# Performance work log

Hardware: AMD Instinct MI355X
Metric: run time of the kernel (lower is better)

The kernel has to match this reference:

```python
import jax, jax.numpy as jnp
import numpy as np

T, B, NN = 20, 4, 500            # timesteps, batch, nodes per sample
M = B * NN                        # big-batched node count = 2000
IN_D, H, H2, OUT = 2, 128, 64, 32


def setup_inputs() -> dict:
    key = jax.random.key(0)
    ks = jax.random.split(key, 16)
    positions = jax.random.normal(ks[0], (T, M, IN_D), jnp.float32)
    adjacency = (jax.random.uniform(ks[1], (T, M, M)) < 0.01).astype(jnp.float32)
    adjacency = adjacency * (1.0 - jnp.eye(M, dtype=jnp.float32))
    ego_mask = jax.random.bernoulli(ks[2], 0.8, (B, T, NN))
    s = lambda k, shp, fan: (jax.random.normal(k, shp, jnp.float32) / np.sqrt(fan)).astype(jnp.float32)
    return {
        'positions': positions,
        'adjacency': adjacency,
        'ego_mask': ego_mask,
        'W1': s(ks[3], (IN_D, H), IN_D), 'b1': jnp.zeros((H,), jnp.float32),
        'W2': s(ks[4], (H, H), H),       'b2': jnp.zeros((H,), jnp.float32),
        'W_ih': s(ks[5], (4 * H, H), H), 'W_hh': s(ks[6], (4 * H, H), H),
        'b_ih': jnp.zeros((4 * H,), jnp.float32), 'b_hh': jnp.zeros((4 * H,), jnp.float32),
        'fc1_w': s(ks[7], (H, H2), H),   'fc1_b': jnp.zeros((H2,), jnp.float32),
        'fc2_w': s(ks[8], (H2, OUT), H2), 'fc2_b': jnp.zeros((OUT,), jnp.float32),
    }


def _forward(positions, adjacency, ego_mask, W1, b1, W2, b2,
             W_ih, W_hh, b_ih, b_hh, fc1_w, fc1_b, fc2_w, fc2_b):
    # ego_mask [B,T,NN] -> [T, B*NN] (matches permute(1,0,2).reshape(T,-1))
    mask = jnp.transpose(ego_mask, (1, 0, 2)).reshape(T, M).astype(positions.dtype)

    def gcn_timestep(x_t, a_t, m_t):
        # masked subgraph + self loops on kept nodes (PyG GCNConv normalization)
        Ahat = a_t * m_t[:, None] * m_t[None, :] + jnp.diag(m_t)   # [M,M]
        deg = Ahat.sum(axis=0)                                      # in-degree (col sum)
        dinv = jnp.where(deg > 0, jax.lax.rsqrt(jnp.maximum(deg, 1e-12)), 0.0)
        An = dinv[:, None] * Ahat * dinv[None, :]                   # D^-1/2 Ahat D^-1/2
        h1 = jax.nn.relu(An.T @ (x_t @ W1) + b1)                    # GCN1 + relu
        h2 = (An.T @ (h1 @ W2) + b2) * m_t[:, None]                 # GCN2, scatter into zeros
        return h2

    placeholder = jax.vmap(gcn_timestep)(positions, adjacency, mask)  # [T, M, H]

    # torch nn.LSTM (batch_first=False) on placeholder.transpose(0,1):
    # sequence axis = nodes (M), batch axis = T
    xs = jnp.transpose(placeholder, (1, 0, 2))  # [M, T, H]

    def lstm_step(carry, x_s):
        h, c = carry
        gates = x_s @ W_ih.T + b_ih + h @ W_hh.T + b_hh
        i, f, g, o = jnp.split(gates, 4, axis=-1)
        c = jax.nn.sigmoid(f) * c + jax.nn.sigmoid(i) * jnp.tanh(g)
        h = jax.nn.sigmoid(o) * jnp.tanh(c)
        return (h, c), h

    init = (jnp.zeros((T, H), positions.dtype), jnp.zeros((T, H), positions.dtype))
    _, lstm_out = jax.lax.scan(lstm_step, init, xs)  # [M, T, H]

    emb = lstm_out.reshape(B, NN, T, H)              # view(B, max_nodes, T, H)
    emb = jax.nn.relu(emb @ fc1_w + fc1_b)
    return emb @ fc2_w + fc2_b                       # [B, NN, T, OUT]


def reference(positions, adjacency, ego_mask, W1, b1, W2, b2,
              W_ih, W_hh, b_ih, b_hh, fc1_w, fc1_b, fc2_w, fc2_b):
    return _forward(positions, adjacency, ego_mask, W1, b1, W2, b2,
                    W_ih, W_hh, b_ih, b_hh, fc1_w, fc1_b, fc2_w, fc2_b)
```

## Files before the change

kernel.cpp:

```cpp
#include <hip/hip_runtime.h>
#include <hip/hip_bf16.h>

#define T_   20
#define B_   4
#define NN_  500
#define M_   2000
#define TM_  40000
#define H_   128
#define G_   512
#define H2_  64
#define OUT_ 32
#define ECAP 64
#define TG_  (T_ * G_)

typedef unsigned short ushort_t;
typedef unsigned int   uint_t;
typedef _Float16       f16;
typedef f16 f16x2 __attribute__((ext_vector_type(2)));
typedef f16 f16x8 __attribute__((ext_vector_type(8)));
typedef float f32x4 __attribute__((ext_vector_type(4)));

#if defined(__has_builtin)
#  if __has_builtin(__builtin_amdgcn_fdot2)
#    define HAVE_FDOT2 1
#  endif
#endif

__device__ inline float fdot2_(f16x2 a, f16x2 b, float c) {
#ifdef HAVE_FDOT2
    return __builtin_amdgcn_fdot2(a, b, c, false);
#else
    return c + (float)a.x * (float)b.x + (float)a.y * (float)b.y;
#endif
}

__device__ inline float fast_sig(float x) {
    float e = __builtin_amdgcn_exp2f(x * -1.4426950408889634f);
    return __builtin_amdgcn_rcpf(1.f + e);
}
__device__ inline float fast_tanh(float x) {
    float e = __builtin_amdgcn_exp2f(x * 2.8853900817779268f);
    return 1.f - 2.f * __builtin_amdgcn_rcpf(e + 1.f);
}

#define BARRAW() asm volatile("s_barrier" ::: "memory")

#define DPPADD(v, ctrl)                                                       \
    do {                                                                      \
        int nb_ = __builtin_amdgcn_update_dpp(                                \
            0, __builtin_bit_cast(int, v), (ctrl), 0xF, 0xF, true);           \
        v += __builtin_bit_cast(float, nb_);                                  \
    } while (0)

__global__ __launch_bounds__(1024) void k0_mask(const void* __restrict__ ego,
                                                float* __restrict__ mf,
                                                int* __restrict__ ecnt) {
    __shared__ int fl[3];
    int tid = threadIdx.x;
    if (tid < 3) fl[tid] = 0;
    __syncthreads();
    const uint_t* dw = (const uint_t*)ego;
    int a = 0, b = 0, c = 0;
    for (int i = tid; i < 2500; i += 1024) {
        uint_t v = dw[i];
        bool isf32  = (v == 0x3F800000u);
        bool isbf16 = (v == 0x00003F80u) || (v == 0x3F803F80u);
        if (isf32)  a = 1;
        if (isbf16) b = 1;
        if (v > 1u && !isf32 && !isbf16) c = 1;
    }
    if (a) fl[0] = 1;
    if (b) fl[1] = 1;
    if (c) fl[2] = 1;
    __syncthreads();
    int mode;
    if (fl[1])      mode = 3;
    else if (fl[0]) mode = 2;
    else if (fl[2]) mode = 1;
    else            mode = 0;
    int e = blockIdx.x * 1024 + tid;
    if (e >= TM_) return;
    ecnt[e] = 0;
    int t = e / M_, i = e % M_;
    int bb = i / NN_, n = i % NN_;
    int src = (bb * T_ + t) * NN_ + n;
    bool on;
    if (mode == 0)      on = ((const int*)ego)[src] != 0;
    else if (mode == 1) on = ((const unsigned char*)ego)[src] != 0;
    else if (mode == 2) on = ((const float*)ego)[src] != 0.f;
    else                on = ((const ushort_t*)ego)[src] != 0;
    mf[e] = on ? 1.f : 0.f;
}

#define JSTRIP 200
__global__ void k1_scan(const float* __restrict__ adj, const float* __restrict__ mf,
                        int* __restrict__ ecnt, int* __restrict__ edges) {
    __shared__ float ms[JSTRIP];
    int t = blockIdx.y, j0 = blockIdx.z * JSTRIP;
    int i = blockIdx.x * 256 + threadIdx.x;
    for (int idx = threadIdx.x; idx < JSTRIP; idx += 256)
        ms[idx] = mf[t * M_ + j0 + idx];
    __syncthreads();
    if (i >= M_) return;
    if (mf[t * M_ + i] == 0.f) return;
    const float* ap = adj + (size_t)t * M_ * M_ + (size_t)j0 * M_ + i;
    int r = t * M_ + i;
    int* ep = edges + (size_t)r * ECAP;
#pragma unroll 8
    for (int jj = 0; jj < JSTRIP; ++jj) {
        float av = ap[(size_t)jj * M_];
        if (av != 0.f && ms[jj] != 0.f) {
            int pos = atomicAdd(&ecnt[r], 1);
            if (pos < ECAP) ep[pos] = j0 + jj;
        }
    }
}

__global__ void k2_y1(const float* __restrict__ pos, const float* __restrict__ W1,
                      const float* __restrict__ mf, const int* __restrict__ ecnt,
                      float* __restrict__ dinv, f16* __restrict__ Y1) {
    int gid = blockIdx.x * 256 + threadIdx.x;
    int r = gid >> 7, h = gid & 127;
    if (r >= TM_) return;
    float mr = mf[r];
    int cnt = ecnt[r];
    float dv = (mr != 0.f) ? __frsqrt_rn((float)(cnt + 1)) : 0.f;
    if (h == 0) dinv[r] = dv;
    float2 xy = ((const float2*)pos)[r];
    float v = xy.x * W1[h] + xy.y * W1[H_ + h];
    Y1[gid] = (f16)(dv * v);
}

__global__ __launch_bounds__(64) void k3_agg1(const f16* __restrict__ Y1,
        const float* __restrict__ dinv, const int* __restrict__ ecnt,
        const int* __restrict__ edges, const float* __restrict__ b1,
        f16* __restrict__ h1) {
    int r = blockIdx.x, q = threadIdx.x;
    int t = r / M_, base = t * M_;
    const uint_t* Yu = (const uint_t*)Y1;
    f16x2 sp = __builtin_bit_cast(f16x2, Yu[(size_t)r * 64 + q]);
    float a0 = (float)sp.x, a1 = (float)sp.y;
    int ec = ecnt[r]; if (ec > ECAP) ec = ECAP;
    const int4* ep4 = (const int4*)(edges + (size_t)r * ECAP);
    for (int e = 0; e < ec; e += 4) {
        int4 ix = ep4[e >> 2];
        int j1 = (e + 1 < ec) ? ix.y : ix.x;
        int j2 = (e + 2 < ec) ? ix.z : ix.x;
        int j3 = (e + 3 < ec) ? ix.w : ix.x;
        uint_t u0 = Yu[(size_t)(base + ix.x) * 64 + q];
        uint_t u1 = Yu[(size_t)(base + j1) * 64 + q];
        uint_t u2 = Yu[(size_t)(base + j2) * 64 + q];
        uint_t u3 = Yu[(size_t)(base + j3) * 64 + q];
        f16x2 p0 = __builtin_bit_cast(f16x2, u0);
        a0 += (float)p0.x; a1 += (float)p0.y;
        if (e + 1 < ec) { f16x2 p = __builtin_bit_cast(f16x2, u1); a0 += (float)p.x; a1 += (float)p.y; }
        if (e + 2 < ec) { f16x2 p = __builtin_bit_cast(f16x2, u2); a0 += (float)p.x; a1 += (float)p.y; }
        if (e + 3 < ec) { f16x2 p = __builtin_bit_cast(f16x2, u3); a0 += (float)p.x; a1 += (float)p.y; }
    }
    float dv = dinv[r];
    float o0 = dv * a0 + b1[2 * q];
    float o1 = dv * a1 + b1[2 * q + 1];
    f16x2 op; op.x = (f16)fmaxf(o0, 0.f); op.y = (f16)fmaxf(o1, 0.f);
    ((uint_t*)h1)[(size_t)r * 64 + q] = __builtin_bit_cast(uint_t, op);
}

__global__ __launch_bounds__(64) void k5_agg2(const f16* __restrict__ Y2,
        const float* __restrict__ dinv, const float* __restrict__ mf,
        const int* __restrict__ ecnt, const int* __restrict__ edges,
        const float* __restrict__ b2, f16* __restrict__ ph) {
    int r = blockIdx.x, q = threadIdx.x;
    int t = r / M_, base = t * M_;
    const uint_t* Yu = (const uint_t*)Y2;
    f16x2 sp = __builtin_bit_cast(f16x2, Yu[(size_t)r * 64 + q]);
    float a0 = (float)sp.x, a1 = (float)sp.y;
    int ec = ecnt[r]; if (ec > ECAP) ec = ECAP;
    const int4* ep4 = (const int4*)(edges + (size_t)r * ECAP);
    for (int e = 0; e < ec; e += 4) {
        int4 ix = ep4[e >> 2];
        int j1 = (e + 1 < ec) ? ix.y : ix.x;
        int j2 = (e + 2 < ec) ? ix.z : ix.x;
        int j3 = (e + 3 < ec) ? ix.w : ix.x;
        uint_t u0 = Yu[(size_t)(base + ix.x) * 64 + q];
        uint_t u1 = Yu[(size_t)(base + j1) * 64 + q];
        uint_t u2 = Yu[(size_t)(base + j2) * 64 + q];
        uint_t u3 = Yu[(size_t)(base + j3) * 64 + q];
        f16x2 p0 = __builtin_bit_cast(f16x2, u0);
        a0 += (float)p0.x; a1 += (float)p0.y;
        if (e + 1 < ec) { f16x2 p = __builtin_bit_cast(f16x2, u1); a0 += (float)p.x; a1 += (float)p.y; }
        if (e + 2 < ec) { f16x2 p = __builtin_bit_cast(f16x2, u2); a0 += (float)p.x; a1 += (float)p.y; }
        if (e + 3 < ec) { f16x2 p = __builtin_bit_cast(f16x2, u3); a0 += (float)p.x; a1 += (float)p.y; }
    }
    float dv = dinv[r], mr = mf[r];
    f16x2 op;
    op.x = (f16)((dv * a0 + b2[2 * q]) * mr);
    op.y = (f16)((dv * a1 + b2[2 * q + 1]) * mr);
    ((uint_t*)ph)[(size_t)r * 64 + q] = __builtin_bit_cast(uint_t, op);
}

#define ALD 136
__global__ __launch_bounds__(256) void kgemm_mfma(const f16* __restrict__ A,
        const float* __restrict__ Bw, int bTrans, int Ntot, int mode,
        const float* __restrict__ dinv, const float* __restrict__ ba,
        const float* __restrict__ bb, f16* __restrict__ Out) {
    __shared__ f16 As[64 * ALD];
    __shared__ f16 Bs[64 * ALD];
    int m0 = blockIdx.x * 64;
    int n0 = blockIdx.y * 64;
    int tid = threadIdx.x;
#pragma unroll
    for (int u = 0; u < 4; ++u) {
        int idx = u * 256 + tid;
        int row = idx >> 4, seg = idx & 15;
        *(f16x8*)&As[row * ALD + seg * 8] =
            *(const f16x8*)(A + (size_t)(m0 + row) * H_ + seg * 8);
    }
    if (bTrans) {
#pragma unroll
        for (int u = 0; u < 16; ++u) {
            int idx = u * 256 + tid;
            int n = idx >> 6, k2 = (idx & 63) * 2;
            float2 v = *(const float2*)(Bw + (size_t)(n0 + n) * H_ + k2);
            f16x2 pk; pk.x = (f16)v.x; pk.y = (f16)v.y;
            *(uint_t*)&Bs[n * ALD + k2] = __builtin_bit_cast(uint_t, pk);
        }
    } else {
#pragma unroll
        for (int u = 0; u < 16; ++u) {
            int idx = u * 256 + tid;
            int n = idx >> 6, k2 = (idx & 63) * 2;
            f16x2 pk;
            pk.x = (f16)Bw[(size_t)k2 * Ntot + n0 + n];
            pk.y = (f16)Bw[(size_t)(k2 + 1) * Ntot + n0 + n];
            *(uint_t*)&Bs[n * ALD + k2] = __builtin_bit_cast(uint_t, pk);
        }
    }
    __syncthreads();
    int w = tid >> 6, lane = tid & 63;
    int col = lane & 15, quad = lane >> 4;
    f32x4 acc[4] = {};
#pragma unroll
    for (int kk = 0; kk < 4; ++kk) {
        f16x8 af = *(const f16x8*)&As[(w * 16 + col) * ALD + kk * 32 + quad * 8];
#pragma unroll
        for (int nt = 0; nt < 4; ++nt) {
            f16x8 bf = *(const f16x8*)&Bs[(nt * 16 + col) * ALD + kk * 32 + quad * 8];
            acc[nt] = __builtin_amdgcn_mfma_f32_16x16x32_f16(af, bf, acc[nt], 0, 0, 0);
        }
    }
    if (mode == 0) {
        float dv[4];
#pragma unroll
        for (int reg = 0; reg < 4; ++reg)
            dv[reg] = dinv[m0 + w * 16 + quad * 4 + reg];
#pragma unroll
        for (int nt = 0; nt < 4; ++nt) {
            int n = n0 + nt * 16 + col;
#pragma unroll
            for (int reg = 0; reg < 4; ++reg) {
                int r = m0 + w * 16 + quad * 4 + reg;
                Out[(size_t)r * Ntot + n] = (f16)(dv[reg] * acc[nt][reg]);
            }
        }
    } else {
#pragma unroll
        for (int nt = 0; nt < 4; ++nt) {
            int n = n0 + nt * 16 + col;
            float bias = ba[n] + bb[n];
            int pos = (n & 127) * 4 + (n >> 7);
#pragma unroll
            for (int reg = 0; reg < 4; ++reg) {
                int r = m0 + w * 16 + quad * 4 + reg;
                int t = r / M_, s = r % M_;
                Out[((size_t)s * T_ + t) * G_ + pos] = (f16)(acc[nt][reg] + bias);
            }
        }
    }
}

__global__ __launch_bounds__(512, 2) void k7_lstm(const float* __restrict__ Whh,
        const f16* __restrict__ xg, f16* __restrict__ lo) {
    __shared__ ushort_t hb2[2][H_];
    int t = blockIdx.x, tid = threadIdx.x;
    int m = tid >> 2, q = tid & 3;
    f16x2 wv[4][16];
#pragma unroll
    for (int gt = 0; gt < 4; ++gt) {
        const float* wr = Whh + (size_t)(gt * H_ + m) * H_ + q * 32;
#pragma unroll
        for (int d = 0; d < 16; ++d) {
            f16x2 p; p.x = (f16)wr[2 * d]; p.y = (f16)wr[2 * d + 1];
            wv[gt][d] = p;
        }
    }
    if (tid < H_) hb2[0][tid] = 0;
    float cst = 0.f;
    const ushort_t* xpu = (const ushort_t*)xg + t * G_ + m * 4 + q;
    ushort_t xa[8], xb[8];
#pragma unroll
    for (int k = 0; k < 8; ++k) xa[k] = xpu[(size_t)k * TG_];
    __syncthreads();

#define LSTM_STEP(S, XV)                                                      \
    do {                                                                      \
        const ushort_t* hp = &hb2[(S) & 1][q * 32];                           \
        uint4 u0 = ((const uint4*)hp)[0];                                     \
        uint4 u1 = ((const uint4*)hp)[1];                                     \
        uint4 u2 = ((const uint4*)hp)[2];                                     \
        uint4 u3 = ((const uint4*)hp)[3];                                     \
        uint_t hu[16] = {u0.x, u0.y, u0.z, u0.w, u1.x, u1.y, u1.z, u1.w,      \
                         u2.x, u2.y, u2.z, u2.w, u3.x, u3.y, u3.z, u3.w};     \
        float a0 = 0.f, a1 = 0.f, a2 = 0.f, a3 = 0.f;                         \
        _Pragma("unroll")                                                     \
        for (int d = 0; d < 16; ++d) {                                        \
            f16x2 e = __builtin_bit_cast(f16x2, hu[d]);                       \
            a0 = fdot2_(wv[0][d], e, a0);                                     \
            a1 = fdot2_(wv[1][d], e, a1);                                     \
            a2 = fdot2_(wv[2][d], e, a2);                                     \
            a3 = fdot2_(wv[3][d], e, a3);                                     \
        }                                                                     \
        float xf = (float)__builtin_bit_cast(f16, (ushort_t)(XV));            \
        a0 += (q == 0) ? xf : 0.f;                                            \
        a1 += (q == 1) ? xf : 0.f;                                            \
        a2 += (q == 2) ? xf : 0.f;                                            \
        a3 += (q == 3) ? xf : 0.f;                                            \
        DPPADD(a0, 0xB1); DPPADD(a0, 0x4E);                                   \
        DPPADD(a1, 0xB1); DPPADD(a1, 0x4E);                                   \
        DPPADD(a2, 0xB1); DPPADD(a2, 0x4E);                                   \
        DPPADD(a3, 0xB1); DPPADD(a3, 0x4E);                                   \
        float gi = fast_sig(a0), gf = fast_sig(a1);                           \
        float gg = fast_tanh(a2), go = fast_sig(a3);                          \
        cst = gf * cst + gi * gg;                                             \
        float hv_ = go * fast_tanh(cst);                                      \
        f16 hh = (f16)hv_;                                                    \
        if (q == 0) {                                                         \
            hb2[((S) & 1) ^ 1][m] = __builtin_bit_cast(ushort_t, hh);         \
            lo[((size_t)(S) * T_ + t) * H_ + m] = hh;                         \
        }                                                                     \
        BARRAW();                                                             \
    } while (0)

    for (int c2 = 0; c2 < 125; ++c2) {
        int s0 = c2 * 16;
#pragma unroll
        for (int k = 0; k < 8; ++k) xb[k] = xpu[(size_t)(s0 + 8 + k) * TG_];
#pragma unroll
        for (int k = 0; k < 8; ++k) LSTM_STEP(s0 + k, xa[k]);
        int nbs = (s0 + 16 <= M_ - 8) ? s0 + 16 : M_ - 8;
#pragma unroll
        for (int k = 0; k < 8; ++k) xa[k] = xpu[(size_t)(nbs + k) * TG_];
#pragma unroll
        for (int k = 0; k < 8; ++k) LSTM_STEP(s0 + 8 + k, xb[k]);
    }
#undef LSTM_STEP
}

__global__ __launch_bounds__(256) void k8_fc(const f16* __restrict__ lo,
        const float* __restrict__ w1, const float* __restrict__ fb1,
        const float* __restrict__ w2, const float* __restrict__ fb2,
        float* __restrict__ out) {
    __shared__ uint_t hl[4][H_ / 2];
    __shared__ float o1f[4][H2_];
    int tid = threadIdx.x;
    int o = tid & 63, rr = tid >> 6;
    f16x2 w1c[64];
#pragma unroll
    for (int d = 0; d < 64; ++d) {
        f16x2 p;
        p.x = (f16)w1[(2 * d) * H2_ + o];
        p.y = (f16)w1[(2 * d + 1) * H2_ + o];
        w1c[d] = p;
    }
    int o2 = o & 31;
    float w2f[64];
#pragma unroll
    for (int d = 0; d < 64; ++d) w2f[d] = w2[d * OUT_ + o2];
    float fb1v = fb1[o], fb2v = fb2[o2];

    for (int r0 = blockIdx.x * 4; r0 < TM_; r0 += 512 * 4) {
        {
            int row = tid >> 6, qq = tid & 63;
            hl[row][qq] = ((const uint_t*)lo)[(size_t)(r0 + row) * 64 + qq];
        }
        __syncthreads();
        float acc = fb1v;
        const uint4* hb = (const uint4*)&hl[rr][0];
#pragma unroll
        for (int d = 0; d < 16; ++d) {
            uint4 hv = hb[d];
            acc = fdot2_(w1c[4 * d + 0], __builtin_bit_cast(f16x2, hv.x), acc);
            acc = fdot2_(w1c[4 * d + 1], __builtin_bit_cast(f16x2, hv.y), acc);
            acc = fdot2_(w1c[4 * d + 2], __builtin_bit_cast(f16x2, hv.z), acc);
            acc = fdot2_(w1c[4 * d + 3], __builtin_bit_cast(f16x2, hv.w), acc);
        }
        o1f[rr][o] = fmaxf(acc, 0.f);
        __syncthreads();
        if (o < OUT_) {
            float a2 = fb2v;
            const float4* ob = (const float4*)&o1f[rr][0];
#pragma unroll
            for (int d = 0; d < 16; ++d) {
                float4 v = ob[d];
                a2 += v.x * w2f[4 * d + 0] + v.y * w2f[4 * d + 1]
                    + v.z * w2f[4 * d + 2] + v.w * w2f[4 * d + 3];
            }
            out[(size_t)(r0 + rr) * OUT_ + o] = a2;
        }
        __syncthreads();
    }
}

extern "C" void kernel_launch(void* const* d_in, const int* in_sizes, int n_in,
                              void* d_out, int out_size, void* d_ws, size_t ws_size,
                              hipStream_t stream) {
    const float* positions = (const float*)d_in[0];
    const float* adjacency = (const float*)d_in[1];
    const void*  ego       = d_in[2];
    const float* W1   = (const float*)d_in[3];
    const float* b1   = (const float*)d_in[4];
    const float* W2   = (const float*)d_in[5];
    const float* b2   = (const float*)d_in[6];
    const float* W_ih = (const float*)d_in[7];
    const float* W_hh = (const float*)d_in[8];
    const float* b_ih = (const float*)d_in[9];
    const float* b_hh = (const float*)d_in[10];
    const float* fc1w = (const float*)d_in[11];
    const float* fc1b = (const float*)d_in[12];
    const float* fc2w = (const float*)d_in[13];
    const float* fc2b = (const float*)d_in[14];
    float* out = (float*)d_out;

    char* p = (char*)d_ws;
    auto alloc = [&](size_t bytes) {
        void* r = (void*)p;
        p += (bytes + 255) & ~(size_t)255;
        return r;
    };
    float* mf    = (float*)alloc((size_t)TM_ * 4);
    float* dinv  = (float*)alloc((size_t)TM_ * 4);
    int*   ecnt  = (int*)alloc((size_t)TM_ * 4);
    int*   edges = (int*)alloc((size_t)TM_ * ECAP * 4);
    f16*   bufC  = (f16*)alloc((size_t)TM_ * H_ * 2);
    f16*   bufD  = (f16*)alloc((size_t)TM_ * H_ * 2);
    f16*   xg    = (f16*)alloc((size_t)TM_ * G_ * 2);
    f16*   Y1 = bufC, *Y2 = bufC;
    f16*   h1 = bufD, *ph = bufD;
    f16*   lo = (f16*)edges;

    hipLaunchKernelGGL(k0_mask, dim3(40), dim3(1024), 0, stream, ego, mf, ecnt);
    hipLaunchKernelGGL(k1_scan, dim3(8, 20, 10), dim3(256), 0, stream,
                       adjacency, mf, ecnt, edges);
    hipLaunchKernelGGL(k2_y1, dim3(20000), dim3(256), 0, stream,
                       positions, W1, mf, ecnt, dinv, Y1);
    hipLaunchKernelGGL(k3_agg1, dim3(40000), dim3(64), 0, stream,
                       Y1, dinv, ecnt, edges, b1, h1);
    hipLaunchKernelGGL(kgemm_mfma, dim3(625, 2), dim3(256), 0, stream,
                       h1, W2, 0, 128, 0, dinv, (const float*)nullptr,
                       (const float*)nullptr, Y2);
    hipLaunchKernelGGL(k5_agg2, dim3(40000), dim3(64), 0, stream,
                       Y2, dinv, mf, ecnt, edges, b2, ph);
    hipLaunchKernelGGL(kgemm_mfma, dim3(625, 8), dim3(256), 0, stream,
                       ph, W_ih, 1, 512, 1, dinv, b_ih, b_hh, xg);
    hipLaunchKernelGGL(k7_lstm, dim3(20), dim3(512), 0, stream, W_hh, xg, lo);
    hipLaunchKernelGGL(k8_fc, dim3(512), dim3(256), 0, stream,
                       lo, fc1w, fc1b, fc2w, fc2b, out);
}
```

Before: 1.776 ms.

## Vectorize adjacency scan, pack aggregation rows per block, grid-stride Y1 kernel

The adjacency scan now has each thread read a float4 covering four destination columns, which cuts thread count and widens loads. The y1 kernel becomes grid-stride over fewer blocks. The two aggregation kernels now process four rows per 256-thread block instead of one row per 64-thread block. The LSTM kernel gets a waves_per_eu attribute. These changes aim to reduce launch and scheduling overhead and to improve memory throughput on the dense adjacency read, at the cost of lower parallelism in the scan and possible imbalance from divergent edge counts within a block.

```diff
diff --git a/kernel.cpp b/kernel.cpp
--- a/kernel.cpp
+++ b/kernel.cpp
@@ -93,49 +93,69 @@
 }
 
 #define JSTRIP 200
-__global__ void k1_scan(const float* __restrict__ adj, const float* __restrict__ mf,
+__global__ __launch_bounds__(256) void k1_scan(const float* __restrict__ adj,
+                        const float* __restrict__ mf,
                         int* __restrict__ ecnt, int* __restrict__ edges) {
     __shared__ float ms[JSTRIP];
     int t = blockIdx.y, j0 = blockIdx.z * JSTRIP;
-    int i = blockIdx.x * 256 + threadIdx.x;
+    int g = blockIdx.x * 256 + threadIdx.x;
     for (int idx = threadIdx.x; idx < JSTRIP; idx += 256)
         ms[idx] = mf[t * M_ + j0 + idx];
     __syncthreads();
-    if (i >= M_) return;
-    if (mf[t * M_ + i] == 0.f) return;
-    const float* ap = adj + (size_t)t * M_ * M_ + (size_t)j0 * M_ + i;
-    int r = t * M_ + i;
-    int* ep = edges + (size_t)r * ECAP;
+    if (g >= M_ / 4) return;
+    int i0 = g * 4;
+    float m0 = mf[t * M_ + i0],     m1 = mf[t * M_ + i0 + 1];
+    float m2 = mf[t * M_ + i0 + 2], m3 = mf[t * M_ + i0 + 3];
+    if (m0 == 0.f && m1 == 0.f && m2 == 0.f && m3 == 0.f) return;
+    const float* ap = adj + (size_t)t * M_ * M_ + (size_t)j0 * M_ + i0;
 #pragma unroll 8
     for (int jj = 0; jj < JSTRIP; ++jj) {
-        float av = ap[(size_t)jj * M_];
-        if (av != 0.f && ms[jj] != 0.f) {
-            int pos = atomicAdd(&ecnt[r], 1);
-            if (pos < ECAP) ep[pos] = j0 + jj;
-        }
-    }
-}
-
-__global__ void k2_y1(const float* __restrict__ pos, const float* __restrict__ W1,
+        float4 av = *(const float4*)(ap + (size_t)jj * M_);
+        float msj = ms[jj];
+        if (msj != 0.f) {
+            if (av.x != 0.f && m0 != 0.f) {
+                int pos = atomicAdd(&ecnt[t * M_ + i0], 1);
+                if (pos < ECAP) edges[(size_t)(t * M_ + i0) * ECAP + pos] = j0 + jj;
+            }
+            if (av.y != 0.f && m1 != 0.f) {
+                int pos = atomicAdd(&ecnt[t * M_ + i0 + 1], 1);
+                if (pos < ECAP) edges[(size_t)(t * M_ + i0 + 1) * ECAP + pos] = j0 + jj;
+            }
+            if (av.z != 0.f && m2 != 0.f) {
+                int pos = atomicAdd(&ecnt[t * M_ + i0 + 2], 1);
+                if (pos < ECAP) edges[(size_t)(t * M_ + i0 + 2) * ECAP + pos] = j0 + jj;
+            }
+            if (av.w != 0.f && m3 != 0.f) {
+                int pos = atomicAdd(&ecnt[t * M_ + i0 + 3], 1);
+                if (pos < ECAP) edges[(size_t)(t * M_ + i0 + 3) * ECAP + pos] = j0 + jj;
+            }
+        }
+    }
+}
+
+__global__ __launch_bounds__(256) void k2_y1(const float* __restrict__ pos,
+                      const float* __restrict__ W1,
                       const float* __restrict__ mf, const int* __restrict__ ecnt,
                       float* __restrict__ dinv, f16* __restrict__ Y1) {
-    int gid = blockIdx.x * 256 + threadIdx.x;
-    int r = gid >> 7, h = gid & 127;
-    if (r >= TM_) return;
-    float mr = mf[r];
-    int cnt = ecnt[r];
-    float dv = (mr != 0.f) ? __frsqrt_rn((float)(cnt + 1)) : 0.f;
-    if (h == 0) dinv[r] = dv;
-    float2 xy = ((const float2*)pos)[r];
-    float v = xy.x * W1[h] + xy.y * W1[H_ + h];
-    Y1[gid] = (f16)(dv * v);
-}
-
-__global__ __launch_bounds__(64) void k3_agg1(const f16* __restrict__ Y1,
+    for (int gid = blockIdx.x * 256 + threadIdx.x; gid < TM_ * H_;
+         gid += 2560 * 256) {
+        int r = gid >> 7, h = gid & 127;
+        float mr = mf[r];
+        int cnt = ecnt[r];
+        float dv = (mr != 0.f) ? __frsqrt_rn((float)(cnt + 1)) : 0.f;
+        if (h == 0) dinv[r] = dv;
+        float2 xy = ((const float2*)pos)[r];
+        float v = xy.x * W1[h] + xy.y * W1[H_ + h];
+        Y1[gid] = (f16)(dv * v);
+    }
+}
+
+__global__ __launch_bounds__(256) void k3_agg1(const f16* __restrict__ Y1,
         const float* __restrict__ dinv, const int* __restrict__ ecnt,
         const int* __restrict__ edges, const float* __restrict__ b1,
         f16* __restrict__ h1) {
-    int r = blockIdx.x, q = threadIdx.x;
+    int r = blockIdx.x * 4 + (threadIdx.x >> 6);
+    int q = threadIdx.x & 63;
     int t = r / M_, base = t * M_;
     const uint_t* Yu = (const uint_t*)Y1;
     f16x2 sp = __builtin_bit_cast(f16x2, Yu[(size_t)r * 64 + q]);
@@ -164,11 +184,12 @@
     ((uint_t*)h1)[(size_t)r * 64 + q] = __builtin_bit_cast(uint_t, op);
 }
 
-__global__ __launch_bounds__(64) void k5_agg2(const f16* __restrict__ Y2,
+__global__ __launch_bounds__(256) void k5_agg2(const f16* __restrict__ Y2,
         const float* __restrict__ dinv, const float* __restrict__ mf,
         const int* __restrict__ ecnt, const int* __restrict__ edges,
         const float* __restrict__ b2, f16* __restrict__ ph) {
-    int r = blockIdx.x, q = threadIdx.x;
+    int r = blockIdx.x * 4 + (threadIdx.x >> 6);
+    int q = threadIdx.x & 63;
     int t = r / M_, base = t * M_;
     const uint_t* Yu = (const uint_t*)Y2;
     f16x2 sp = __builtin_bit_cast(f16x2, Yu[(size_t)r * 64 + q]);
@@ -277,8 +298,10 @@
     }
 }
 
-__global__ __launch_bounds__(512, 2) void k7_lstm(const float* __restrict__ Whh,
-        const f16* __restrict__ xg, f16* __restrict__ lo) {
+__global__ __launch_bounds__(512, 2)
+__attribute__((amdgpu_waves_per_eu(2, 2)))
+void k7_lstm(const float* __restrict__ Whh,
+             const f16* __restrict__ xg, f16* __restrict__ lo) {
     __shared__ ushort_t hb2[2][H_];
     int t = blockIdx.x, tid = threadIdx.x;
     int m = tid >> 2, q = tid & 3;
@@ -447,16 +470,16 @@
     f16*   lo = (f16*)edges;
 
     hipLaunchKernelGGL(k0_mask, dim3(40), dim3(1024), 0, stream, ego, mf, ecnt);
-    hipLaunchKernelGGL(k1_scan, dim3(8, 20, 10), dim3(256), 0, stream,
+    hipLaunchKernelGGL(k1_scan, dim3(2, 20, 10), dim3(256), 0, stream,
                        adjacency, mf, ecnt, edges);
-    hipLaunchKernelGGL(k2_y1, dim3(20000), dim3(256), 0, stream,
+    hipLaunchKernelGGL(k2_y1, dim3(2560), dim3(256), 0, stream,
                        positions, W1, mf, ecnt, dinv, Y1);
-    hipLaunchKernelGGL(k3_agg1, dim3(40000), dim3(64), 0, stream,
+    hipLaunchKernelGGL(k3_agg1, dim3(10000), dim3(256), 0, stream,
                        Y1, dinv, ecnt, edges, b1, h1);
     hipLaunchKernelGGL(kgemm_mfma, dim3(625, 2), dim3(256), 0, stream,
                        h1, W2, 0, 128, 0, dinv, (const float*)nullptr,
                        (const float*)nullptr, Y2);
-    hipLaunchKernelGGL(k5_agg2, dim3(40000), dim3(64), 0, stream,
+    hipLaunchKernelGGL(k5_agg2, dim3(10000), dim3(256), 0, stream,
                        Y2, dinv, mf, ecnt, edges, b2, ph);
     hipLaunchKernelGGL(kgemm_mfma, dim3(625, 8), dim3(256), 0, stream,
                        ph, W_ih, 1, 512, 1, dinv, b_ih, b_hh, xg);
```

Result: slower. 1.853 ms (+4.4%).
